# Optimization experiments

Hardware: AMD Instinct MI355X
Metric: run time of the kernel (lower is better)

The kernel has to match this reference:

```python
import jax, jax.numpy as jnp
import numpy as np

B, R, T, D = 256, 36, 64, 1024
EPS_L2 = 1e-8   # lavse l2norm eps
EPS_BN = 1e-5   # torch BatchNorm1d default
LEAK = 0.1      # LeakyReLU slope in ClippedL2Norm


def l2norm(x, axis):
    n = jnp.sqrt(jnp.sum(x * x, axis=axis, keepdims=True)) + EPS_L2
    return x / n


def setup_inputs() -> dict:
    key = jax.random.key(0)
    k1, k2, k3, k4, k5, k6, k7 = jax.random.split(key, 7)
    img_embed = jax.random.normal(k1, (B, R, D), dtype=jnp.float32)
    cap_embed = jax.random.normal(k2, (B, T, D), dtype=jnp.float32)
    lens = jax.random.randint(k3, (B,), 1, T + 1, dtype=jnp.int32)  # at least 1 word
    # nn.Linear(D, 2D): weight (2D, D), bias (2D,)
    lim = 1.0 / np.sqrt(D)
    fc_w = jax.random.uniform(k4, (2 * D, D), jnp.float32, -lim, lim)
    fc_b = jax.random.uniform(k5, (2 * D,), jnp.float32, -lim, lim)
    # BatchNorm1d(D) affine params
    bn_w = jnp.ones((D,), jnp.float32)
    bn_b = jnp.zeros((D,), jnp.float32)
    return {"img_embed": img_embed, "cap_embed": cap_embed, "lens": lens,
            "fc_w": fc_w, "fc_b": fc_b, "bn_w": bn_w, "bn_b": bn_b}


def reference(img_embed, cap_embed, lens, fc_w, fc_b, bn_w, bn_b):
    # permute to channel-first: (B, D, T) / (B, D, R)
    cap = jnp.transpose(cap_embed, (0, 2, 1))
    img = jnp.transpose(img_embed, (0, 2, 1))
    # ClippedL2Norm: leaky relu then l2-normalize along last (token/region) axis
    cap = l2norm(jax.nn.leaky_relu(cap, LEAK), axis=2)
    img = l2norm(jax.nn.leaky_relu(img, LEAK), axis=2)

    t = cap.shape[2]
    mask = (jnp.arange(t)[None, :] < lens[:, None]).astype(cap.dtype)  # (B, T)
    # ragged mean pooling over valid words: (B, D)
    cap_mean = jnp.einsum('bdt,bt->bd', cap, mask) / lens[:, None].astype(cap.dtype)

    # fc(cap).view(D, 2): interleaved alphas/betas
    params = (cap_mean @ fc_w.T + fc_b).reshape(-1, cap.shape[1], 2)  # (B, D, 2)
    alphas, betas = params[..., 0], params[..., 1]                    # (B, D) each

    # BatchNorm1d over (B, D, R) in training mode (batch stats, biased var) — hoisted
    mu = jnp.mean(img, axis=(0, 2))
    var = jnp.mean((img - mu[None, :, None]) ** 2, axis=(0, 2))
    bn = (img - mu[None, :, None]) * (bn_w / jnp.sqrt(var + EPS_BN))[None, :, None] \
         + bn_b[None, :, None]
    base = bn.mean(-1)  # (B_img, D); mean commutes with per-channel affine

    # caption-conditioned affine modulation: (B_cap, B_img, D)
    img_vec = base[None, :, :] * alphas[:, None, :] + betas[:, None, :]
    img_vec = l2norm(img_vec, axis=-1)
    cap_vec = l2norm(cap_mean, axis=-1)  # (B_cap, D)

    # sims[img_j, cap_i] = <img_vec[i, j], cap_vec[i]>
    sims = jnp.einsum('cbd,cd->bc', img_vec, cap_vec)
    return sims
```

## Files before the change

kernel.cpp:

```cpp
#include <hip/hip_runtime.h>
#include <hip/hip_bf16.h>

#define B_ 256
#define R_ 36
#define T_ 64
#define D_ 1024

#define SWZ64(k, c) ((c) ^ ((((k) >> 4) & 3) << 4))
#define SWZ32(k, b) ((b) ^ ((((k) >> 3) & 3) << 3))

__device__ __forceinline__ float lrelu(float x) { return x >= 0.0f ? x : 0.1f * x; }

__device__ __forceinline__ float block_sum(float v, float* sred) {
#pragma unroll
  for (int off = 32; off > 0; off >>= 1) v += __shfl_down(v, off, 64);
  int w = threadIdx.x >> 6;
  if ((threadIdx.x & 63) == 0) sred[w] = v;
  __syncthreads();
  float r = sred[0] + sred[1] + sred[2] + sred[3];
  __syncthreads();
  return r;
}

__global__ __launch_bounds__(256) void input_kernel(const float* __restrict__ cap,
    const float* __restrict__ img, const int* __restrict__ lens,
    float* __restrict__ cap_mean, float* __restrict__ rowsum, float* __restrict__ rowss) {
  int bid = blockIdx.x;
  if (bid < 512) {
    int b = bid >> 1;
    int d0 = (bid & 1) * 512 + threadIdx.x * 2;
    int len = lens[b];
    const float* src = cap + (size_t)b * (T_ * D_) + d0;
    float s20 = 0.f, s21 = 0.f, sm0 = 0.f, sm1 = 0.f;
#pragma unroll 8
    for (int tt = 0; tt < T_; ++tt) {
      float2 v = *(const float2*)&src[(size_t)tt * D_];
      float y0 = lrelu(v.x), y1 = lrelu(v.y);
      s20 += y0 * y0; s21 += y1 * y1;
      bool in = tt < len;
      sm0 += in ? y0 : 0.0f;
      sm1 += in ? y1 : 0.0f;
    }
    float il = 1.0f / (float)len;
    float2 cm;
    cm.x = sm0 / (sqrtf(s20) + 1e-8f) * il;
    cm.y = sm1 / (sqrtf(s21) + 1e-8f) * il;
    *(float2*)&cap_mean[(size_t)b * D_ + d0] = cm;
  } else {
    int b = (bid - 512) >> 1;
    int d0 = ((bid - 512) & 1) * 512 + threadIdx.x * 2;
    const float* src = img + (size_t)b * (R_ * D_) + d0;
    float s10 = 0.f, s11 = 0.f, s20 = 0.f, s21 = 0.f;
#pragma unroll 6
    for (int r = 0; r < R_; ++r) {
      float2 v = *(const float2*)&src[(size_t)r * D_];
      float y0 = lrelu(v.x), y1 = lrelu(v.y);
      s10 += y0; s11 += y1;
      s20 += y0 * y0; s21 += y1 * y1;
    }
    float n0 = sqrtf(s20) + 1e-8f, n1 = sqrtf(s21) + 1e-8f;
    float2 rs, ss;
    rs.x = s10 / n0; rs.y = s11 / n1;
    ss.x = s20 / (n0 * n0); ss.y = s21 / (n1 * n1);
    *(float2*)&rowsum[(size_t)b * D_ + d0] = rs;
    *(float2*)&rowss[(size_t)b * D_ + d0] = ss;
  }
}

__global__ __launch_bounds__(256) void gemm_stats_kernel(
    const float* __restrict__ cap_mean, const float* __restrict__ fc_w,
    const float* __restrict__ rowsum, const float* __restrict__ rowss,
    const float* __restrict__ bn_w, const float* __restrict__ bn_b,
    float* __restrict__ Ppart, float* __restrict__ g, float* __restrict__ h) {
  __shared__ float As[32][64];
  __shared__ float Bs[32][64];
  __shared__ float s1[4][64], s2[4][64];
  int bid = blockIdx.x;
  int t = threadIdx.x;
  if (bid < 512) {
    int nt = bid & 31, ct = (bid >> 5) & 3, kz = bid >> 7;
    int tr = t >> 4, tc = t & 15;
    int cs = t >> 2, k0 = (t & 3) << 3;
    const float* arow = cap_mean + (size_t)(ct * 64 + cs) * D_ + kz * 256;
    const float* brow = fc_w + (size_t)(nt * 64 + cs) * D_ + kz * 256;
    float acc[4][4] = {};
    int sa = SWZ64(k0, cs);
    for (int kb = 0; kb < 256; kb += 32) {
      float4 a0 = *(const float4*)&arow[kb + k0];
      float4 a1 = *(const float4*)&arow[kb + k0 + 4];
      float4 b0 = *(const float4*)&brow[kb + k0];
      float4 b1 = *(const float4*)&brow[kb + k0 + 4];
      __syncthreads();
      As[k0 + 0][sa] = a0.x; As[k0 + 1][sa] = a0.y; As[k0 + 2][sa] = a0.z; As[k0 + 3][sa] = a0.w;
      As[k0 + 4][sa] = a1.x; As[k0 + 5][sa] = a1.y; As[k0 + 6][sa] = a1.z; As[k0 + 7][sa] = a1.w;
      Bs[k0 + 0][sa] = b0.x; Bs[k0 + 1][sa] = b0.y; Bs[k0 + 2][sa] = b0.z; Bs[k0 + 3][sa] = b0.w;
      Bs[k0 + 4][sa] = b1.x; Bs[k0 + 5][sa] = b1.y; Bs[k0 + 6][sa] = b1.z; Bs[k0 + 7][sa] = b1.w;
      __syncthreads();
#pragma unroll
      for (int kk = 0; kk < 32; ++kk) {
        float4 av = *(const float4*)&As[kk][SWZ64(kk, tr * 4)];
        float4 bv = *(const float4*)&Bs[kk][SWZ64(kk, tc * 4)];
        acc[0][0] += av.x * bv.x; acc[0][1] += av.x * bv.y; acc[0][2] += av.x * bv.z; acc[0][3] += av.x * bv.w;
        acc[1][0] += av.y * bv.x; acc[1][1] += av.y * bv.y; acc[1][2] += av.y * bv.z; acc[1][3] += av.y * bv.w;
        acc[2][0] += av.z * bv.x; acc[2][1] += av.z * bv.y; acc[2][2] += av.z * bv.z; acc[2][3] += av.z * bv.w;
        acc[3][0] += av.w * bv.x; acc[3][1] += av.w * bv.y; acc[3][2] += av.w * bv.z; acc[3][3] += av.w * bv.w;
      }
    }
    int c = ct * 64 + tr * 4;
    int n = nt * 64 + tc * 4;
#pragma unroll
    for (int i = 0; i < 4; ++i) {
      *(float4*)&Ppart[((size_t)kz * 256 + c + i) * 2048 + n] =
          make_float4(acc[i][0], acc[i][1], acc[i][2], acc[i][3]);
    }
  } else {
    int sb = bid - 512;
    int dl = t & 63;
    int d = sb * 64 + dl;
    int bg = t >> 6;
    float cs = 0.0f, c2 = 0.0f;
    for (int b = bg * 64; b < bg * 64 + 64; ++b) {
      cs += rowsum[(size_t)b * D_ + d];
      c2 += rowss[(size_t)b * D_ + d];
    }
    s1[bg][dl] = cs;
    s2[bg][dl] = c2;
    __syncthreads();
    if (t < 64) {
      cs = s1[0][dl] + s1[1][dl] + s1[2][dl] + s1[3][dl];
      c2 = s2[0][dl] + s2[1][dl] + s2[2][dl] + s2[3][dl];
      const float inv = 1.0f / (float)(B_ * R_);
      float m = cs * inv, ex2 = c2 * inv;
      float var = ex2 - m * m;
      float gg = bn_w[d] / sqrtf(var + 1e-5f);
      g[d] = gg;
      h[d] = m * gg - bn_b[d];
    }
  }
}

__global__ __launch_bounds__(256) void reduce_scal_kernel(const float* __restrict__ Ppart,
    const float* __restrict__ fc_b, const float* __restrict__ cap_mean,
    float* __restrict__ params, float* __restrict__ rawC, float* __restrict__ BBc,
    float* __restrict__ rn) {
  __shared__ float sred[4], sred2[4], sred3[4];
  int c = blockIdx.x, t = threadIdx.x;
  float4 p0 = reinterpret_cast<const float4*>(fc_b)[2 * t];
  float4 p1 = reinterpret_cast<const float4*>(fc_b)[2 * t + 1];
#pragma unroll
  for (int kz = 0; kz < 4; ++kz) {
    size_t base4 = ((size_t)kz * 256 + c) * 512;
    float4 q0 = reinterpret_cast<const float4*>(Ppart)[base4 + 2 * t];
    float4 q1 = reinterpret_cast<const float4*>(Ppart)[base4 + 2 * t + 1];
    p0.x += q0.x; p0.y += q0.y; p0.z += q0.z; p0.w += q0.w;
    p1.x += q1.x; p1.y += q1.y; p1.z += q1.z; p1.w += q1.w;
  }
  reinterpret_cast<float4*>(params)[(size_t)c * 512 + 2 * t] = p0;
  reinterpret_cast<float4*>(params)[(size_t)c * 512 + 2 * t + 1] = p1;
  float4 cm = reinterpret_cast<const float4*>(cap_mean)[(size_t)c * 256 + t];
  float sBc = p0.y * cm.x + p0.w * cm.y + p1.y * cm.z + p1.w * cm.w;
  float sB2 = p0.y * p0.y + p0.w * p0.w + p1.y * p1.y + p1.w * p1.w;
  float scm = cm.x * cm.x + cm.y * cm.y + cm.z * cm.z + cm.w * cm.w;
  float a = block_sum(sBc, sred);
  float bsum = block_sum(sB2, sred2);
  float cq = block_sum(scm, sred3);
  if (t == 0) {
    rawC[c] = a;
    BBc[c] = bsum;
    rn[c] = 1.0f / (sqrtf(cq) + 1e-8f);
  }
}

__global__ __launch_bounds__(256) void sims_kernel(const float* __restrict__ rowsum,
    const float* __restrict__ g, const float* __restrict__ h,
    const float* __restrict__ params, const float* __restrict__ cap_mean,
    float* __restrict__ Npart, float* __restrict__ Qpart) {
  __shared__ float Tb[64][32];
  __shared__ float Tacv[64][64];
  __shared__ float Ta2[64][64];
  __shared__ float Tab[64][64];
  int t = threadIdx.x;
  int bt = blockIdx.x, ct = blockIdx.y, kz = blockIdx.z;
  int k0 = kz * 64;
  int tr = t >> 4, tc = t & 15;
  int bb = t >> 3, kb = (t & 7) << 3;
  int cc = t >> 2, dc = (t & 3) << 4;
  const float* prow = params + (size_t)(ct * 64 + cc) * 2048 + 2 * k0;
  const float* cmrow = cap_mean + (size_t)(ct * 64 + cc) * 1024 + k0;
  const float* rsrow = rowsum + (size_t)(bt * 32 + bb) * 1024 + k0;
  const float invR = 1.0f / (float)R_;
  {
    float4 v0 = *(const float4*)&rsrow[kb];
    float4 v1 = *(const float4*)&rsrow[kb + 4];
    float4 g0 = *(const float4*)&g[k0 + kb];
    float4 g1 = *(const float4*)&g[k0 + kb + 4];
    float4 h0 = *(const float4*)&h[k0 + kb];
    float4 h1 = *(const float4*)&h[k0 + kb + 4];
    int sb = SWZ32(kb, bb);
    Tb[kb + 0][sb] = v0.x * invR * g0.x - h0.x;
    Tb[kb + 1][sb] = v0.y * invR * g0.y - h0.y;
    Tb[kb + 2][sb] = v0.z * invR * g0.z - h0.z;
    Tb[kb + 3][sb] = v0.w * invR * g0.w - h0.w;
    Tb[kb + 4][sb] = v1.x * invR * g1.x - h1.x;
    Tb[kb + 5][sb] = v1.y * invR * g1.y - h1.y;
    Tb[kb + 6][sb] = v1.z * invR * g1.z - h1.z;
    Tb[kb + 7][sb] = v1.w * invR * g1.w - h1.w;
  }
  int sc = SWZ64(dc, cc);
#pragma unroll
  for (int j = 0; j < 16; j += 4) {
    int d = dc + j;
    float4 p0 = *(const float4*)&prow[2 * d];
    float4 p1 = *(const float4*)&prow[2 * d + 4];
    float4 cm = *(const float4*)&cmrow[d];
    Tacv[d + 0][sc] = p0.x * cm.x; Ta2[d + 0][sc] = p0.x * p0.x; Tab[d + 0][sc] = 2.f * p0.x * p0.y;
    Tacv[d + 1][sc] = p0.z * cm.y; Ta2[d + 1][sc] = p0.z * p0.z; Tab[d + 1][sc] = 2.f * p0.z * p0.w;
    Tacv[d + 2][sc] = p1.x * cm.z; Ta2[d + 2][sc] = p1.x * p1.x; Tab[d + 2][sc] = 2.f * p1.x * p1.y;
    Tacv[d + 3][sc] = p1.z * cm.w; Ta2[d + 3][sc] = p1.z * p1.z; Tab[d + 3][sc] = 2.f * p1.z * p1.w;
  }
  __syncthreads();
  float accN[2][4] = {};
  float accQ[2][4] = {};
#pragma unroll 8
  for (int kk = 0; kk < 64; ++kk) {
    float2 bv = *(const float2*)&Tb[kk][SWZ32(kk, tr * 2)];
    float4 acv = *(const float4*)&Tacv[kk][SWZ64(kk, tc * 4)];
    float4 a2v = *(const float4*)&Ta2[kk][SWZ64(kk, tc * 4)];
    float4 abv = *(const float4*)&Tab[kk][SWZ64(kk, tc * 4)];
    float b0 = bv.x, b1 = bv.y;
    float q0 = b0 * b0, q1 = b1 * b1;
    accN[0][0] += b0 * acv.x; accN[0][1] += b0 * acv.y; accN[0][2] += b0 * acv.z; accN[0][3] += b0 * acv.w;
    accN[1][0] += b1 * acv.x; accN[1][1] += b1 * acv.y; accN[1][2] += b1 * acv.z; accN[1][3] += b1 * acv.w;
    accQ[0][0] += q0 * a2v.x; accQ[0][1] += q0 * a2v.y; accQ[0][2] += q0 * a2v.z; accQ[0][3] += q0 * a2v.w;
    accQ[1][0] += q1 * a2v.x; accQ[1][1] += q1 * a2v.y; accQ[1][2] += q1 * a2v.z; accQ[1][3] += q1 * a2v.w;
    accQ[0][0] += b0 * abv.x; accQ[0][1] += b0 * abv.y; accQ[0][2] += b0 * abv.z; accQ[0][3] += b0 * abv.w;
    accQ[1][0] += b1 * abv.x; accQ[1][1] += b1 * abv.y; accQ[1][2] += b1 * abv.z; accQ[1][3] += b1 * abv.w;
  }
  int br = bt * 32 + tr * 2;
  int c = ct * 64 + tc * 4;
#pragma unroll
  for (int i = 0; i < 2; ++i) {
    size_t o = ((size_t)kz * 256 + br + i) * 256 + c;
    *(float4*)&Npart[o] = make_float4(accN[i][0], accN[i][1], accN[i][2], accN[i][3]);
    *(float4*)&Qpart[o] = make_float4(accQ[i][0], accQ[i][1], accQ[i][2], accQ[i][3]);
  }
}

__global__ __launch_bounds__(256) void final_kernel(const float* __restrict__ Npart,
    const float* __restrict__ Qpart, const float* __restrict__ rawC,
    const float* __restrict__ BBc, const float* __restrict__ rn, float* __restrict__ out) {
  int b = blockIdx.x, c = threadIdx.x;
  float N = rawC[c], Q = BBc[c];
#pragma unroll
  for (int kz = 0; kz < 16; ++kz) {
    size_t o = ((size_t)kz * 256 + b) * 256 + c;
    N += Npart[o];
    Q += Qpart[o];
  }
  out[b * 256 + c] = N * rn[c] / (sqrtf(Q) + 1e-8f);
}

extern "C" void kernel_launch(void* const* d_in, const int* in_sizes, int n_in,
                              void* d_out, int out_size, void* d_ws, size_t ws_size,
                              hipStream_t stream) {
  const float* img = (const float*)d_in[0];
  const float* cap = (const float*)d_in[1];
  const int* lens = (const int*)d_in[2];
  const float* fc_w = (const float*)d_in[3];
  const float* fc_b = (const float*)d_in[4];
  const float* bn_w = (const float*)d_in[5];
  const float* bn_b = (const float*)d_in[6];
  float* out = (float*)d_out;
  float* ws = (float*)d_ws;

  float* cap_mean = ws;
  float* rowsum   = ws + 262144;
  float* rowss    = ws + 524288;
  float* g        = ws + 786432;
  float* h        = ws + 787456;
  float* params   = ws + 788480;
  float* rawC     = ws + 1312768;
  float* BBc      = ws + 1313024;
  float* rn       = ws + 1313280;
  float* region   = ws + 1313536;
  float* Ppart    = region;
  float* Npart    = region;
  float* Qpart    = region + 1048576;

  input_kernel<<<1024, 256, 0, stream>>>(cap, img, lens, cap_mean, rowsum, rowss);
  gemm_stats_kernel<<<528, 256, 0, stream>>>(cap_mean, fc_w, rowsum, rowss,
                                             bn_w, bn_b, Ppart, g, h);
  reduce_scal_kernel<<<256, 256, 0, stream>>>(Ppart, fc_b, cap_mean, params,
                                              rawC, BBc, rn);
  sims_kernel<<<dim3(8, 4, 16), 256, 0, stream>>>(rowsum, g, h, params, cap_mean,
                                                  Npart, Qpart);
  final_kernel<<<256, 256, 0, stream>>>(Npart, Qpart, rawC, BBc, rn, out);
}
```

Measured before the change: 64.69 us.

## Vectorize input reduction with float4 and retile fc GEMM to 64x128 with split-K 8

The input kernel now uses 512-thread blocks, one per batch row. Each thread loads float4 and handles half the token/region rows, and the two halves are combined through shared memory. The fc GEMM tile grows to 64x128 with 4x8 per-thread accumulators and K split 8 ways, so reduce_scal sums eight partials. This aims at wider memory accesses and more FMA work per shared-memory load, at the cost of a larger partial-product buffer in the workspace and an extra shared-memory reduction.

```diff
diff --git a/kernel.cpp b/kernel.cpp
--- a/kernel.cpp
+++ b/kernel.cpp
@@ -8,6 +8,7 @@
 
 #define SWZ64(k, c) ((c) ^ ((((k) >> 4) & 3) << 4))
 #define SWZ32(k, b) ((b) ^ ((((k) >> 3) & 3) << 3))
+#define SWZA(k, c)  ((c) ^ ((((k) >> 2) & 3) << 4))
 
 __device__ __forceinline__ float lrelu(float x) { return x >= 0.0f ? x : 0.1f * x; }
 
@@ -22,48 +23,69 @@
   return r;
 }
 
-__global__ __launch_bounds__(256) void input_kernel(const float* __restrict__ cap,
+__global__ __launch_bounds__(512) void input_kernel(const float* __restrict__ cap,
     const float* __restrict__ img, const int* __restrict__ lens,
     float* __restrict__ cap_mean, float* __restrict__ rowsum, float* __restrict__ rowss) {
+  __shared__ float4 redA[256], redB[256];
   int bid = blockIdx.x;
-  if (bid < 512) {
-    int b = bid >> 1;
-    int d0 = (bid & 1) * 512 + threadIdx.x * 2;
+  int t = threadIdx.x;
+  int rp = t >> 8, dq = t & 255;
+  if (bid < 256) {
+    int b = bid;
     int len = lens[b];
-    const float* src = cap + (size_t)b * (T_ * D_) + d0;
-    float s20 = 0.f, s21 = 0.f, sm0 = 0.f, sm1 = 0.f;
+    const float4* src = reinterpret_cast<const float4*>(cap) + (size_t)b * (T_ * D_ / 4) + dq;
+    float4 s2 = {0, 0, 0, 0}, sm = {0, 0, 0, 0};
 #pragma unroll 8
-    for (int tt = 0; tt < T_; ++tt) {
-      float2 v = *(const float2*)&src[(size_t)tt * D_];
-      float y0 = lrelu(v.x), y1 = lrelu(v.y);
-      s20 += y0 * y0; s21 += y1 * y1;
+    for (int it = 0; it < 32; ++it) {
+      int tt = it * 2 + rp;
+      float4 v = src[(size_t)tt * 256];
+      float y0 = lrelu(v.x), y1 = lrelu(v.y), y2 = lrelu(v.z), y3 = lrelu(v.w);
+      s2.x += y0 * y0; s2.y += y1 * y1; s2.z += y2 * y2; s2.w += y3 * y3;
       bool in = tt < len;
-      sm0 += in ? y0 : 0.0f;
-      sm1 += in ? y1 : 0.0f;
-    }
-    float il = 1.0f / (float)len;
-    float2 cm;
-    cm.x = sm0 / (sqrtf(s20) + 1e-8f) * il;
-    cm.y = sm1 / (sqrtf(s21) + 1e-8f) * il;
-    *(float2*)&cap_mean[(size_t)b * D_ + d0] = cm;
+      sm.x += in ? y0 : 0.0f; sm.y += in ? y1 : 0.0f;
+      sm.z += in ? y2 : 0.0f; sm.w += in ? y3 : 0.0f;
+    }
+    if (rp) { redA[dq] = s2; redB[dq] = sm; }
+    __syncthreads();
+    if (!rp) {
+      float4 o2 = redA[dq], om = redB[dq];
+      s2.x += o2.x; s2.y += o2.y; s2.z += o2.z; s2.w += o2.w;
+      sm.x += om.x; sm.y += om.y; sm.z += om.z; sm.w += om.w;
+      float il = 1.0f / (float)len;
+      float4 cm;
+      cm.x = sm.x / (sqrtf(s2.x) + 1e-8f) * il;
+      cm.y = sm.y / (sqrtf(s2.y) + 1e-8f) * il;
+      cm.z = sm.z / (sqrtf(s2.z) + 1e-8f) * il;
+      cm.w = sm.w / (sqrtf(s2.w) + 1e-8f) * il;
+      reinterpret_cast<float4*>(cap_mean)[(size_t)b * 256 + dq] = cm;
+    }
   } else {
-    int b = (bid - 512) >> 1;
-    int d0 = ((bid - 512) & 1) * 512 + threadIdx.x * 2;
-    const float* src = img + (size_t)b * (R_ * D_) + d0;
-    float s10 = 0.f, s11 = 0.f, s20 = 0.f, s21 = 0.f;
+    int b = bid - 256;
+    const float4* src = reinterpret_cast<const float4*>(img) + (size_t)b * (R_ * D_ / 4) + dq;
+    float4 s1 = {0, 0, 0, 0}, s2 = {0, 0, 0, 0};
 #pragma unroll 6
-    for (int r = 0; r < R_; ++r) {
-      float2 v = *(const float2*)&src[(size_t)r * D_];
-      float y0 = lrelu(v.x), y1 = lrelu(v.y);
-      s10 += y0; s11 += y1;
-      s20 += y0 * y0; s21 += y1 * y1;
-    }
-    float n0 = sqrtf(s20) + 1e-8f, n1 = sqrtf(s21) + 1e-8f;
-    float2 rs, ss;
-    rs.x = s10 / n0; rs.y = s11 / n1;
-    ss.x = s20 / (n0 * n0); ss.y = s21 / (n1 * n1);
-    *(float2*)&rowsum[(size_t)b * D_ + d0] = rs;
-    *(float2*)&rowss[(size_t)b * D_ + d0] = ss;
+    for (int it = 0; it < 18; ++it) {
+      int r = it * 2 + rp;
+      float4 v = src[(size_t)r * 256];
+      float y0 = lrelu(v.x), y1 = lrelu(v.y), y2 = lrelu(v.z), y3 = lrelu(v.w);
+      s1.x += y0; s1.y += y1; s1.z += y2; s1.w += y3;
+      s2.x += y0 * y0; s2.y += y1 * y1; s2.z += y2 * y2; s2.w += y3 * y3;
+    }
+    if (rp) { redA[dq] = s1; redB[dq] = s2; }
+    __syncthreads();
+    if (!rp) {
+      float4 o1 = redA[dq], o2 = redB[dq];
+      s1.x += o1.x; s1.y += o1.y; s1.z += o1.z; s1.w += o1.w;
+      s2.x += o2.x; s2.y += o2.y; s2.z += o2.z; s2.w += o2.w;
+      float n0 = sqrtf(s2.x) + 1e-8f, n1 = sqrtf(s2.y) + 1e-8f;
+      float n2 = sqrtf(s2.z) + 1e-8f, n3 = sqrtf(s2.w) + 1e-8f;
+      float4 rs, ss;
+      rs.x = s1.x / n0; rs.y = s1.y / n1; rs.z = s1.z / n2; rs.w = s1.w / n3;
+      ss.x = s2.x / (n0 * n0); ss.y = s2.y / (n1 * n1);
+      ss.z = s2.z / (n2 * n2); ss.w = s2.w / (n3 * n3);
+      reinterpret_cast<float4*>(rowsum)[(size_t)b * 256 + dq] = rs;
+      reinterpret_cast<float4*>(rowss)[(size_t)b * 256 + dq] = ss;
+    }
   }
 }
 
@@ -72,46 +94,52 @@
     const float* __restrict__ rowsum, const float* __restrict__ rowss,
     const float* __restrict__ bn_w, const float* __restrict__ bn_b,
     float* __restrict__ Ppart, float* __restrict__ g, float* __restrict__ h) {
-  __shared__ float As[32][64];
-  __shared__ float Bs[32][64];
-  __shared__ float s1[4][64], s2[4][64];
+  __shared__ float As[16][64];
+  __shared__ float Bs[16][128];
+  __shared__ float s1s[4][64], s2s[4][64];
   int bid = blockIdx.x;
   int t = threadIdx.x;
   if (bid < 512) {
-    int nt = bid & 31, ct = (bid >> 5) & 3, kz = bid >> 7;
+    int nt = bid & 15, ct = (bid >> 4) & 3, kz = bid >> 6;
     int tr = t >> 4, tc = t & 15;
-    int cs = t >> 2, k0 = (t & 3) << 3;
-    const float* arow = cap_mean + (size_t)(ct * 64 + cs) * D_ + kz * 256;
-    const float* brow = fc_w + (size_t)(nt * 64 + cs) * D_ + kz * 256;
-    float acc[4][4] = {};
-    int sa = SWZ64(k0, cs);
-    for (int kb = 0; kb < 256; kb += 32) {
-      float4 a0 = *(const float4*)&arow[kb + k0];
-      float4 a1 = *(const float4*)&arow[kb + k0 + 4];
-      float4 b0 = *(const float4*)&brow[kb + k0];
-      float4 b1 = *(const float4*)&brow[kb + k0 + 4];
+    int ca = t >> 2, ka = (t & 3) << 2;
+    int nb = t >> 1, kb0 = (t & 1) << 3;
+    const float* arow = cap_mean + (size_t)(ct * 64 + ca) * D_ + kz * 128;
+    const float* brow = fc_w + (size_t)(nt * 128 + nb) * D_ + kz * 128;
+    float acc[4][8] = {};
+    int sca = SWZA(ka, ca);
+    for (int kb = 0; kb < 128; kb += 16) {
+      float4 av = *(const float4*)&arow[kb + ka];
+      float4 b0 = *(const float4*)&brow[kb + kb0];
+      float4 b1 = *(const float4*)&brow[kb + kb0 + 4];
       __syncthreads();
-      As[k0 + 0][sa] = a0.x; As[k0 + 1][sa] = a0.y; As[k0 + 2][sa] = a0.z; As[k0 + 3][sa] = a0.w;
-      As[k0 + 4][sa] = a1.x; As[k0 + 5][sa] = a1.y; As[k0 + 6][sa] = a1.z; As[k0 + 7][sa] = a1.w;
-      Bs[k0 + 0][sa] = b0.x; Bs[k0 + 1][sa] = b0.y; Bs[k0 + 2][sa] = b0.z; Bs[k0 + 3][sa] = b0.w;
-      Bs[k0 + 4][sa] = b1.x; Bs[k0 + 5][sa] = b1.y; Bs[k0 + 6][sa] = b1.z; Bs[k0 + 7][sa] = b1.w;
+      As[ka + 0][sca] = av.x; As[ka + 1][sca] = av.y;
+      As[ka + 2][sca] = av.z; As[ka + 3][sca] = av.w;
+      Bs[kb0 + 0][nb] = b0.x; Bs[kb0 + 1][nb] = b0.y; Bs[kb0 + 2][nb] = b0.z; Bs[kb0 + 3][nb] = b0.w;
+      Bs[kb0 + 4][nb] = b1.x; Bs[kb0 + 5][nb] = b1.y; Bs[kb0 + 6][nb] = b1.z; Bs[kb0 + 7][nb] = b1.w;
       __syncthreads();
 #pragma unroll
-      for (int kk = 0; kk < 32; ++kk) {
-        float4 av = *(const float4*)&As[kk][SWZ64(kk, tr * 4)];
-        float4 bv = *(const float4*)&Bs[kk][SWZ64(kk, tc * 4)];
-        acc[0][0] += av.x * bv.x; acc[0][1] += av.x * bv.y; acc[0][2] += av.x * bv.z; acc[0][3] += av.x * bv.w;
-        acc[1][0] += av.y * bv.x; acc[1][1] += av.y * bv.y; acc[1][2] += av.y * bv.z; acc[1][3] += av.y * bv.w;
-        acc[2][0] += av.z * bv.x; acc[2][1] += av.z * bv.y; acc[2][2] += av.z * bv.z; acc[2][3] += av.z * bv.w;
-        acc[3][0] += av.w * bv.x; acc[3][1] += av.w * bv.y; acc[3][2] += av.w * bv.z; acc[3][3] += av.w * bv.w;
+      for (int kk = 0; kk < 16; ++kk) {
+        float4 a = *(const float4*)&As[kk][SWZA(kk, tr * 4)];
+        float4 q0 = *(const float4*)&Bs[kk][tc * 8];
+        float4 q1 = *(const float4*)&Bs[kk][tc * 8 + 4];
+        acc[0][0] += a.x * q0.x; acc[0][1] += a.x * q0.y; acc[0][2] += a.x * q0.z; acc[0][3] += a.x * q0.w;
+        acc[0][4] += a.x * q1.x; acc[0][5] += a.x * q1.y; acc[0][6] += a.x * q1.z; acc[0][7] += a.x * q1.w;
+        acc[1][0] += a.y * q0.x; acc[1][1] += a.y * q0.y; acc[1][2] += a.y * q0.z; acc[1][3] += a.y * q0.w;
+        acc[1][4] += a.y * q1.x; acc[1][5] += a.y * q1.y; acc[1][6] += a.y * q1.z; acc[1][7] += a.y * q1.w;
+        acc[2][0] += a.z * q0.x; acc[2][1] += a.z * q0.y; acc[2][2] += a.z * q0.z; acc[2][3] += a.z * q0.w;
+        acc[2][4] += a.z * q1.x; acc[2][5] += a.z * q1.y; acc[2][6] += a.z * q1.z; acc[2][7] += a.z * q1.w;
+        acc[3][0] += a.w * q0.x; acc[3][1] += a.w * q0.y; acc[3][2] += a.w * q0.z; acc[3][3] += a.w * q0.w;
+        acc[3][4] += a.w * q1.x; acc[3][5] += a.w * q1.y; acc[3][6] += a.w * q1.z; acc[3][7] += a.w * q1.w;
       }
     }
     int c = ct * 64 + tr * 4;
-    int n = nt * 64 + tc * 4;
+    int n = nt * 128 + tc * 8;
 #pragma unroll
     for (int i = 0; i < 4; ++i) {
-      *(float4*)&Ppart[((size_t)kz * 256 + c + i) * 2048 + n] =
-          make_float4(acc[i][0], acc[i][1], acc[i][2], acc[i][3]);
+      size_t o = ((size_t)kz * 256 + c + i) * 2048 + n;
+      *(float4*)&Ppart[o] = make_float4(acc[i][0], acc[i][1], acc[i][2], acc[i][3]);
+      *(float4*)&Ppart[o + 4] = make_float4(acc[i][4], acc[i][5], acc[i][6], acc[i][7]);
     }
   } else {
     int sb = bid - 512;
@@ -123,12 +151,12 @@
       cs += rowsum[(size_t)b * D_ + d];
       c2 += rowss[(size_t)b * D_ + d];
     }
-    s1[bg][dl] = cs;
-    s2[bg][dl] = c2;
+    s1s[bg][dl] = cs;
+    s2s[bg][dl] = c2;
     __syncthreads();
     if (t < 64) {
-      cs = s1[0][dl] + s1[1][dl] + s1[2][dl] + s1[3][dl];
-      c2 = s2[0][dl] + s2[1][dl] + s2[2][dl] + s2[3][dl];
+      cs = s1s[0][dl] + s1s[1][dl] + s1s[2][dl] + s1s[3][dl];
+      c2 = s2s[0][dl] + s2s[1][dl] + s2s[2][dl] + s2s[3][dl];
       const float inv = 1.0f / (float)(B_ * R_);
       float m = cs * inv, ex2 = c2 * inv;
       float var = ex2 - m * m;
@@ -148,7 +176,7 @@
   float4 p0 = reinterpret_cast<const float4*>(fc_b)[2 * t];
   float4 p1 = reinterpret_cast<const float4*>(fc_b)[2 * t + 1];
 #pragma unroll
-  for (int kz = 0; kz < 4; ++kz) {
+  for (int kz = 0; kz < 8; ++kz) {
     size_t base4 = ((size_t)kz * 256 + c) * 512;
     float4 q0 = reinterpret_cast<const float4*>(Ppart)[base4 + 2 * t];
     float4 q1 = reinterpret_cast<const float4*>(Ppart)[base4 + 2 * t + 1];
@@ -287,7 +315,7 @@
   float* Npart    = region;
   float* Qpart    = region + 1048576;
 
-  input_kernel<<<1024, 256, 0, stream>>>(cap, img, lens, cap_mean, rowsum, rowss);
+  input_kernel<<<512, 512, 0, stream>>>(cap, img, lens, cap_mean, rowsum, rowss);
   gemm_stats_kernel<<<528, 256, 0, stream>>>(cap_mean, fc_w, rowsum, rowss,
                                              bn_w, bn_b, Ppart, g, h);
   reduce_scal_kernel<<<256, 256, 0, stream>>>(Ppart, fc_b, cap_mean, params,
```

Result: slower. 69.55 us (+7.5%).
